# Optimization experiments

Measured on AMD Instinct MI355X. Metric: run time of the kernel, lower is better.

Reference implementation:

```python
import jax, jax.numpy as jnp
import numpy as np

DIM = 768
HEADS = 12
HEAD_DIM = DIM // HEADS
SCALE = HEAD_DIM ** (-0.5)
GAMMA_INIT = 1.0


def _split_heads(x, B, H, Dh):
    # [B, N, C] -> [B, H, N, Dh]
    return x.reshape(B, -1, H, Dh).transpose(0, 2, 1, 3)


def setup_inputs() -> dict:
    key = jax.random.key(0)
    ks = jax.random.split(key, 10)
    B, N, C = 4, 1024, DIM
    w = lambda k: jax.random.normal(k, (C, C), dtype=jnp.float32) * 0.02
    return {
        "fc": jax.random.normal(ks[0], (B, N, C), dtype=jnp.float32),
        "fs": jax.random.normal(ks[1], (B, N, C), dtype=jnp.float32),
        "Wqc": w(ks[2]),
        "Wqs": w(ks[3]),
        "Wkc": w(ks[4]),
        "Wvc": w(ks[5]),
        "Wvs": w(ks[6]),
        "gamma": jnp.ones((HEADS,), dtype=jnp.float32) * GAMMA_INIT,
        "Wpc": w(ks[7]),
        "bpc": jnp.zeros((C,), dtype=jnp.float32),
        "Wps": w(ks[8]),
        "bps": jnp.zeros((C,), dtype=jnp.float32),
    }


def reference(fc, fs, Wqc, Wqs, Wkc, Wvc, Wvs, gamma, Wpc, bpc, Wps, bps):
    B, N, C = fc.shape
    H, Dh = HEADS, HEAD_DIM
    sg = jax.lax.stop_gradient

    qc = _split_heads(fc @ Wqc, B, H, Dh)
    qs = _split_heads(fs @ Wqs, B, H, Dh)
    kc = _split_heads(fc @ Wkc, B, H, Dh)
    vc = _split_heads(fc @ Wvc, B, H, Dh)
    vs = _split_heads(fs @ Wvs, B, H, Dh)

    # content attention: standard scaled QK^T
    attn_c = jnp.einsum("bhnd,bhmd->bhnm", qc, kc) * SCALE
    # semantic attention: L2-normalized self-similarity, per-head gamma
    qs_n = qs / jnp.linalg.norm(qs, axis=-1, keepdims=True)
    attn_s = jnp.einsum("bhnd,bhmd->bhnm", qs_n, qs_n) * gamma[None, :, None, None]

    # double softmax: identical forward values, asymmetric stop-gradients
    attn1 = jax.nn.softmax(attn_c + sg(attn_s), axis=-1)
    attn2 = jax.nn.softmax(sg(attn_c) + attn_s, axis=-1)

    oc = jnp.einsum("bhnm,bhmd->bhnd", attn1, vc).transpose(0, 2, 1, 3).reshape(B, N, C)
    os_ = jnp.einsum("bhnm,bhmd->bhnd", attn2, vs).transpose(0, 2, 1, 3).reshape(B, N, C)

    out_c = oc @ Wpc + bpc
    out_s = os_ @ Wps + bps
    return (out_c, out_s)
```

## Files before the change

kernel.cpp:

```cpp
#include <hip/hip_runtime.h>
#include <cstdint>
#include <cstddef>

#define DEV __device__ __forceinline__

typedef __bf16 v8bf __attribute__((ext_vector_type(8)));
typedef float v4f __attribute__((ext_vector_type(4)));
typedef float f32x16 __attribute__((ext_vector_type(16)));
typedef uint16_t u16;

DEV u16 f2bf(float f) {
    union { __bf16 b; u16 u; } cv;
    cv.b = (__bf16)f;
    return cv.u;
}

DEV uint32_t pkbf(float a, float b) {
    typedef __bf16 bf2v __attribute__((ext_vector_type(2)));
    union { bf2v v; uint32_t u; } c;
    c.v = (bf2v){(__bf16)a, (__bf16)b};
    return c.u;
}

DEV void gload16(void* lds, const void* g) {
    __builtin_amdgcn_global_load_lds(
        (const __attribute__((address_space(1))) unsigned int*)g,
        (__attribute__((address_space(3))) unsigned int*)lds, 16, 0, 0);
}

DEV void wait_vm0() {
    asm volatile("s_waitcnt vmcnt(0)" ::: "memory");
    __builtin_amdgcn_sched_barrier(0);
}

__global__ __launch_bounds__(256) void k_prep(
    const float* __restrict__ fc, const float* __restrict__ fs,
    u16* __restrict__ fcb, u16* __restrict__ fsb,
    const float* __restrict__ w0, const float* __restrict__ w1, const float* __restrict__ w2,
    const float* __restrict__ w3, const float* __restrict__ w4, const float* __restrict__ w5,
    const float* __restrict__ w6, u16* __restrict__ Wt) {
    __shared__ float tl[32][33];
    int bid = blockIdx.x;
    if (bid < 6144) {
        const float* s = (bid < 3072) ? fc : fs;
        u16* d = (bid < 3072) ? fcb : fsb;
        int blk = (bid < 3072) ? bid : (bid - 3072);
        int i = blk * 256 + threadIdx.x;
        float4 v = reinterpret_cast<const float4*>(s)[i];
        ushort4 o;
        o.x = f2bf(v.x); o.y = f2bf(v.y); o.z = f2bf(v.z); o.w = f2bf(v.w);
        reinterpret_cast<ushort4*>(d)[i] = o;
        return;
    }
    int tid = bid - 6144;
    int z = tid / 576, rem = tid % 576;
    const float* W;
    switch (z) {
        case 0: W = w0; break; case 1: W = w1; break; case 2: W = w2; break;
        case 3: W = w3; break; case 4: W = w4; break; case 5: W = w5; break;
        default: W = w6; break;
    }
    int n0 = (rem % 24) * 32, k0 = (rem / 24) * 32;
    int tx = threadIdx.x & 31, ty = threadIdx.x >> 5;
    #pragma unroll
    for (int i = 0; i < 4; ++i)
        tl[ty + i*8][tx] = W[(size_t)(k0 + ty + i*8) * 768 + n0 + tx];
    __syncthreads();
    u16* O = Wt + (size_t)z * 589824;
    #pragma unroll
    for (int i = 0; i < 4; ++i)
        O[(size_t)(n0 + ty + i*8) * 768 + k0 + tx] = f2bf(tl[tx][ty + i*8]);
}

DEV void gemm_main(const u16* __restrict__ A, const u16* __restrict__ W,
                   u16* As, u16* Bs, int m0, int n0, v4f acc[4][4]) {
    const int t = threadIdx.x, lane = t & 63;
    const int wid = t >> 6, wm = wid >> 1, wn = wid & 1;
    const int lr = lane & 15, kg = lane >> 4;
    const int lrow = lane >> 3, lslot = lane & 7;
    const int s = lslot ^ lrow;
    #pragma unroll
    for (int mi = 0; mi < 4; ++mi)
        #pragma unroll
        for (int ni = 0; ni < 4; ++ni) acc[mi][ni] = (v4f){0.f, 0.f, 0.f, 0.f};
    for (int kt = 0; kt < 12; ++kt) {
        int k0 = kt * 64;
        #pragma unroll
        for (int c = 0; c < 4; ++c) {
            int rb = wid * 32 + c * 8;
            int r = rb + lrow;
            gload16((char*)As + rb * 128, A + (size_t)(m0 + r) * 768 + k0 + s * 8);
            gload16((char*)Bs + rb * 128, W + (size_t)(n0 + r) * 768 + k0 + s * 8);
        }
        __syncthreads();
        #pragma unroll
        for (int kk = 0; kk < 2; ++kk) {
            int kb2 = (kk * 32 + kg * 8) * 2;
            v8bf af[4], bfr[4];
            #pragma unroll
            for (int mi = 0; mi < 4; ++mi) {
                int rr = wm * 64 + mi * 16 + lr;
                af[mi] = *reinterpret_cast<const v8bf*>(reinterpret_cast<const char*>(As) + rr * 128 + (kb2 ^ ((rr & 7) << 4)));
            }
            #pragma unroll
            for (int ni = 0; ni < 4; ++ni) {
                int rr = wn * 64 + ni * 16 + lr;
                bfr[ni] = *reinterpret_cast<const v8bf*>(reinterpret_cast<const char*>(Bs) + rr * 128 + (kb2 ^ ((rr & 7) << 4)));
            }
            #pragma unroll
            for (int mi = 0; mi < 4; ++mi)
                #pragma unroll
                for (int ni = 0; ni < 4; ++ni)
                    acc[mi][ni] = __builtin_amdgcn_mfma_f32_16x16x32_bf16(af[mi], bfr[ni], acc[mi][ni], 0, 0, 0);
        }
        __syncthreads();
    }
}

__global__ __launch_bounds__(256) void k_gemm_proj(
    const u16* __restrict__ fcb, const u16* __restrict__ fsb, const u16* __restrict__ Wt,
    u16* __restrict__ qc, u16* __restrict__ kc, u16* __restrict__ vc,
    u16* __restrict__ qs, u16* __restrict__ vs) {
    __shared__ __align__(16) u16 As[8192], Bs[8192];
    const u16* A; const u16* W; u16* O;
    switch (blockIdx.z) {
        case 0:  A = fcb; W = Wt;              O = qc; break;
        case 1:  A = fcb; W = Wt + 589824;     O = kc; break;
        case 2:  A = fcb; W = Wt + 2 * 589824; O = vc; break;
        case 3:  A = fsb; W = Wt + 3 * 589824; O = qs; break;
        default: A = fsb; W = Wt + 4 * 589824; O = vs; break;
    }
    int m0 = blockIdx.y * 128, n0 = blockIdx.x * 128;
    v4f acc[4][4];
    gemm_main(A, W, As, Bs, m0, n0, acc);
    const int lane = threadIdx.x & 63, wid = threadIdx.x >> 6;
    const int wm = wid >> 1, wn = wid & 1, lr = lane & 15, kg = lane >> 4;
    if (blockIdx.z == 0) {
        #pragma unroll
        for (int mi = 0; mi < 4; ++mi)
            #pragma unroll
            for (int ni = 0; ni < 4; ++ni)
                #pragma unroll
                for (int r = 0; r < 4; ++r) acc[mi][ni][r] *= 0.18033688f;
    } else if (blockIdx.z == 3) {
        #pragma unroll
        for (int mi = 0; mi < 4; ++mi)
            #pragma unroll
            for (int r = 0; r < 4; ++r) {
                float ss = 0.f;
                #pragma unroll
                for (int ni = 0; ni < 4; ++ni) ss += acc[mi][ni][r] * acc[mi][ni][r];
                ss += __shfl_xor(ss, 1); ss += __shfl_xor(ss, 2);
                ss += __shfl_xor(ss, 4); ss += __shfl_xor(ss, 8);
                float rs = rsqrtf(ss);
                #pragma unroll
                for (int ni = 0; ni < 4; ++ni) acc[mi][ni][r] *= rs;
            }
    }
    #pragma unroll
    for (int mi = 0; mi < 4; ++mi)
        #pragma unroll
        for (int ni = 0; ni < 4; ++ni)
            #pragma unroll
            for (int r = 0; r < 4; ++r) {
                int rowg = m0 + wm * 64 + mi * 16 + kg * 4 + r;
                int colg = n0 + wn * 64 + ni * 16 + lr;
                O[(size_t)rowg * 768 + colg] = f2bf(acc[mi][ni][r]);
            }
}

__global__ __launch_bounds__(256) void k_gemm_out(
    const u16* __restrict__ ocb, const u16* __restrict__ osb, const u16* __restrict__ Wt,
    const float* __restrict__ bpc, const float* __restrict__ bps, float* __restrict__ out) {
    __shared__ __align__(16) u16 As[8192], Bs[8192];
    const u16* A; const u16* W; const float* bias; float* O;
    if (blockIdx.z == 0) { A = ocb; W = Wt + 5 * 589824; bias = bpc; O = out; }
    else                 { A = osb; W = Wt + 6 * 589824; bias = bps; O = out + 3145728; }
    int m0 = blockIdx.y * 128, n0 = blockIdx.x * 128;
    v4f acc[4][4];
    gemm_main(A, W, As, Bs, m0, n0, acc);
    const int lane = threadIdx.x & 63, wid = threadIdx.x >> 6;
    const int wm = wid >> 1, wn = wid & 1, lr = lane & 15, kg = lane >> 4;
    #pragma unroll
    for (int mi = 0; mi < 4; ++mi)
        #pragma unroll
        for (int ni = 0; ni < 4; ++ni)
            #pragma unroll
            for (int r = 0; r < 4; ++r) {
                int rowg = m0 + wm * 64 + mi * 16 + kg * 4 + r;
                int colg = n0 + wn * 64 + ni * 16 + lr;
                O[(size_t)rowg * 768 + colg] = acc[mi][ni][r] + bias[colg];
            }
}

__global__ __launch_bounds__(256) void k_transpose_v(
    const u16* __restrict__ vc, const u16* __restrict__ vs,
    u16* __restrict__ vcT, u16* __restrict__ vsT) {
    __shared__ u16 tile[64][65];
    const u16* src = blockIdx.z ? vs : vc;
    u16* dst = blockIdx.z ? vsT : vcT;
    int bh = blockIdx.y, b = bh / 12, h = bh % 12;
    int n0 = blockIdx.x * 64;
    int t = threadIdx.x;
    #pragma unroll
    for (int i = 0; i < 16; ++i) {
        int idx = i * 256 + t, n = idx >> 6, d = idx & 63;
        tile[n][d] = src[(size_t)(b * 1024 + n0 + n) * 768 + h * 64 + d];
    }
    __syncthreads();
    #pragma unroll
    for (int i = 0; i < 16; ++i) {
        int idx = i * 256 + t, d = idx >> 6, n = idx & 63;
        dst[(size_t)(bh * 64 + d) * 1024 + n0 + n] = tile[n][d];
    }
}

__global__ __launch_bounds__(256, 2) void k_attn(
    const u16* __restrict__ qc, const u16* __restrict__ kc, const u16* __restrict__ qsn,
    const u16* __restrict__ vcT, const u16* __restrict__ vsT,
    const float* __restrict__ gamma,
    u16* __restrict__ oc, u16* __restrict__ os) {
    __shared__ __align__(16) u16 SH[24576];
    u16* K_s8  = SH;
    u16* Q2_s8 = SH + 4096;
    u16* Vb    = SH + 8192;
    const int t = threadIdx.x, lane = t & 63, w = t >> 6;
    const int lq = lane & 31, hf = lane >> 5;
    const int qg = w >> 1, kvh = w & 1;
    const int lrow = lane >> 3, lslot = lane & 7;
    const int sslot = lslot ^ lrow;

    int lin = blockIdx.y * 16 + blockIdx.x;
    int swz = (lin & 7) * 96 + (lin >> 3);
    const int qb = swz & 15, bh = swz >> 4;
    const int b = bh / 12, h = bh % 12;
    const float gam = gamma[h] * 1.44269504088896340736f;

    const u16* gb; size_t rstride, kmul;
    switch (w) {
        case 0:  gb = kc  + (size_t)b * 786432 + h * 64; rstride = 768;  kmul = 768; break;
        case 1:  gb = qsn + (size_t)b * 786432 + h * 64; rstride = 768;  kmul = 768; break;
        case 2:  gb = vcT + (size_t)bh * 65536;          rstride = 1024; kmul = 1;   break;
        default: gb = vsT + (size_t)bh * 65536;          rstride = 1024; kmul = 1;   break;
    }
    u16* fixdst = (w == 0) ? K_s8 : Q2_s8;

    const u16* qp1 = qc  + (size_t)(b * 1024 + qb * 64 + qg * 32 + lq) * 768 + h * 64 + hf * 8;
    const u16* qp2 = qsn + (size_t)(b * 1024 + qb * 64 + qg * 32 + lq) * 768 + h * 64 + hf * 8;
    v8bf qcB[4], qsB[4];
    #pragma unroll
    for (int s = 0; s < 4; ++s) {
        qcB[s] = *reinterpret_cast<const v8bf*>(qp1 + s * 16);
        qsB[s] = *reinterpret_cast<const v8bf*>(qp2 + s * 16);
    }

    f32x16 ocA[2], osA[2];
    #pragma unroll
    for (int dt = 0; dt < 2; ++dt) {
        #pragma unroll
        for (int r = 0; r < 16; ++r) { ocA[dt][r] = 0.f; osA[dt][r] = 0.f; }
    }
    float lsum = 0.f;

    {
        char* ld = (w < 2) ? (char*)fixdst : (char*)(Vb + (w - 2) * 4096);
        #pragma unroll
        for (int c = 0; c < 8; ++c) {
            int r = c * 8 + lrow;
            int ss = sslot ^ ((c & 1) << 2);
            gload16(ld + c * 1024, gb + (size_t)r * rstride + ss * 8);
        }
    }
    wait_vm0();
    __builtin_amdgcn_s_barrier();

    int cur = 0;
    for (int tile = 0; tile < 16; ++tile) {
        if (tile < 15 && w >= 2) {
            size_t kv1 = (size_t)(tile + 1) * 64;
            char* ld = (char*)(Vb + ((cur ^ 1) * 2 + (w - 2)) * 4096);
            #pragma unroll
            for (int c = 0; c < 8; ++c) {
                int r = c * 8 + lrow;
                int ss = sslot ^ ((c & 1) << 2);
                gload16(ld + c * 1024, gb + kv1 * kmul + (size_t)r * rstride + ss * 8);
            }
        }
        const char* K_s  = (const char*)K_s8;
        const char* Q2_s = (const char*)Q2_s8;
        const char* Vc_s = (const char*)(Vb + (cur * 2 + 0) * 4096);
        const char* Vs_s = (const char*)(Vb + (cur * 2 + 1) * 4096);

        f32x16 ac, as;
        #pragma unroll
        for (int r = 0; r < 16; ++r) { ac[r] = 0.f; as[r] = 0.f; }
        const int rowA = kvh * 32 + lq;
        const int rswA = ((rowA & 7) << 4) ^ (((rowA >> 3) & 1) << 6);
        __builtin_amdgcn_s_setprio(1);
        #pragma unroll
        for (int s = 0; s < 4; ++s) {
            int colb = s * 32 + hf * 16;
            int off = rowA * 128 + (colb ^ rswA);
            v8bf kf  = *reinterpret_cast<const v8bf*>(K_s + off);
            v8bf q2f = *reinterpret_cast<const v8bf*>(Q2_s + off);
            ac = __builtin_amdgcn_mfma_f32_32x32x16_bf16(kf,  qcB[s], ac, 0, 0, 0);
            as = __builtin_amdgcn_mfma_f32_32x32x16_bf16(q2f, qsB[s], as, 0, 0, 0);
        }
        __builtin_amdgcn_s_setprio(0);

        __builtin_amdgcn_s_barrier();
        if (tile < 15 && w < 2) {
            size_t kv1 = (size_t)(tile + 1) * 64;
            #pragma unroll
            for (int c = 0; c < 8; ++c) {
                int r = c * 8 + lrow;
                int ss = sslot ^ ((c & 1) << 2);
                gload16((char*)fixdst + c * 1024, gb + kv1 * kmul + (size_t)r * rstride + ss * 8);
            }
        }

        float p[16];
        #pragma unroll
        for (int r = 0; r < 16; ++r)
            p[r] = __builtin_exp2f(fmaf(gam, as[r], ac[r]));
        lsum += ((p[0]+p[1])+(p[2]+p[3])) + ((p[4]+p[5])+(p[6]+p[7]))
              + ((p[8]+p[9])+(p[10]+p[11])) + ((p[12]+p[13])+(p[14]+p[15]));

        uint32_t A0 = pkbf(p[0], p[1]),  A1 = pkbf(p[2], p[3]);
        uint32_t A2 = pkbf(p[4], p[5]),  A3 = pkbf(p[6], p[7]);
        uint32_t A4 = pkbf(p[8], p[9]),  A5 = pkbf(p[10], p[11]);
        uint32_t A6 = pkbf(p[12], p[13]), A7 = pkbf(p[14], p[15]);
        uint32_t pay0 = hf ? A0 : A2;
        uint32_t pay1 = hf ? A1 : A3;
        uint32_t rec0 = (uint32_t)__shfl_xor((int)pay0, 32);
        uint32_t rec1 = (uint32_t)__shfl_xor((int)pay1, 32);
        uint32_t w0 = hf ? rec0 : A0;
        uint32_t w1 = hf ? rec1 : A1;
        uint32_t w2 = hf ? A2 : rec0;
        uint32_t w3 = hf ? A3 : rec1;
        uint32_t pay2 = hf ? A4 : A6;
        uint32_t pay3 = hf ? A5 : A7;
        uint32_t rec2 = (uint32_t)__shfl_xor((int)pay2, 32);
        uint32_t rec3 = (uint32_t)__shfl_xor((int)pay3, 32);
        uint32_t w4 = hf ? rec2 : A4;
        uint32_t w5 = hf ? rec3 : A5;
        uint32_t w6 = hf ? A6 : rec2;
        uint32_t w7 = hf ? A7 : rec3;
        union { uint32_t u[4]; v8bf v; } pa0, pa1;
        pa0.u[0] = w0; pa0.u[1] = w1; pa0.u[2] = w2; pa0.u[3] = w3;
        pa1.u[0] = w4; pa1.u[1] = w5; pa1.u[2] = w6; pa1.u[3] = w7;

        __builtin_amdgcn_s_setprio(1);
        #pragma unroll
        for (int dt = 0; dt < 2; ++dt) {
            int rowV = dt * 32 + lq;
            int rswV = ((rowV & 7) << 4) ^ (((rowV >> 3) & 1) << 6);
            #pragma unroll
            for (int s = 0; s < 2; ++s) {
                int colb = kvh * 64 + s * 32 + hf * 16;
                int off = rowV * 128 + (colb ^ rswV);
                v8bf vcf = *reinterpret_cast<const v8bf*>(Vc_s + off);
                v8bf vsf = *reinterpret_cast<const v8bf*>(Vs_s + off);
                v8bf ap = s ? pa1.v : pa0.v;
                ocA[dt] = __builtin_amdgcn_mfma_f32_32x32x16_bf16(ap, vcf, ocA[dt], 0, 0, 0);
                osA[dt] = __builtin_amdgcn_mfma_f32_32x32x16_bf16(ap, vsf, osA[dt], 0, 0, 0);
            }
        }
        __builtin_amdgcn_s_setprio(0);

        wait_vm0();
        __builtin_amdgcn_s_barrier();
        cur ^= 1;
    }

    lsum += __shfl_xor(lsum, 32);
    float* red   = reinterpret_cast<float*>(SH);
    float* red_l = red;
    float* red_o = red + 64;
    if (kvh == 1) {
        if (lane < 32) red_l[qg * 32 + lq] = lsum;
        #pragma unroll
        for (int st = 0; st < 2; ++st)
            #pragma unroll
            for (int dt = 0; dt < 2; ++dt)
                #pragma unroll
                for (int r = 0; r < 16; ++r) {
                    int idx = st * 32 + dt * 16 + r;
                    float v = st ? osA[dt][r] : ocA[dt][r];
                    red_o[(qg * 64 + idx) * 64 + lane] = v;
                }
    }
    __syncthreads();
    if (kvh == 0) {
        float ltot = lsum + red_l[qg * 32 + lq];
        float rl = 1.0f / ltot;
        if (lane < 32) red_l[qg * 32 + lq] = rl;
        #pragma unroll
        for (int st = 0; st < 2; ++st)
            #pragma unroll
            for (int dt = 0; dt < 2; ++dt)
                #pragma unroll
                for (int r = 0; r < 16; ++r) {
                    int rowq = (r & 3) + 8 * (r >> 2) + 4 * hf;
                    float rlv = red_l[qg * 32 + rowq];
                    int idx = st * 32 + dt * 16 + r;
                    float own = st ? osA[dt][r] : ocA[dt][r];
                    float v = (own + red_o[(qg * 64 + idx) * 64 + lane]) * rlv;
                    u16* dst = st ? os : oc;
                    dst[(size_t)(b * 1024 + qb * 64 + qg * 32 + rowq) * 768 + h * 64 + dt * 32 + lq] = f2bf(v);
                }
    }
}

extern "C" void kernel_launch(void* const* d_in, const int* in_sizes, int n_in,
                              void* d_out, int out_size, void* d_ws, size_t ws_size,
                              hipStream_t stream) {
    const float* fc    = (const float*)d_in[0];
    const float* fs    = (const float*)d_in[1];
    const float* Wqc   = (const float*)d_in[2];
    const float* Wqs   = (const float*)d_in[3];
    const float* Wkc   = (const float*)d_in[4];
    const float* Wvc   = (const float*)d_in[5];
    const float* Wvs   = (const float*)d_in[6];
    const float* gamma = (const float*)d_in[7];
    const float* Wpc   = (const float*)d_in[8];
    const float* bpc   = (const float*)d_in[9];
    const float* Wps   = (const float*)d_in[10];
    const float* bps   = (const float*)d_in[11];
    float* out = (float*)d_out;

    const size_t NT = 3145728;
    u16* ws  = (u16*)d_ws;
    u16* fcb = ws;
    u16* fsb = fcb + NT;
    u16* Wt  = fsb + NT;
    u16* qc  = Wt + (size_t)7 * 589824;
    u16* kc  = qc + NT;
    u16* vc  = kc + NT;
    u16* qs  = vc + NT;
    u16* vs  = qs + NT;
    u16* vcT = vs + NT;
    u16* vsT = vcT + NT;
    u16* ocb = fcb;
    u16* osb = fsb;

    k_prep<<<10176, 256, 0, stream>>>(fc, fs, fcb, fsb, Wqc, Wkc, Wvc, Wqs, Wvs, Wpc, Wps, Wt);
    k_gemm_proj<<<dim3(6, 32, 5), 256, 0, stream>>>(fcb, fsb, Wt, qc, kc, vc, qs, vs);
    k_transpose_v<<<dim3(16, 48, 2), 256, 0, stream>>>(vc, vs, vcT, vsT);
    k_attn<<<dim3(16, 48), 256, 0, stream>>>(qc, kc, qs, vcT, vsT, gamma, ocb, osb);
    k_gemm_out<<<dim3(6, 32, 2), 256, 0, stream>>>(ocb, osb, Wt, bpc, bps, out);
}
```

Measured before the change: 125.3 us.

## Fuse V transpose into projection GEMM epilogue and swizzle GEMM tile order

The separate V-transpose kernel is removed. The projection GEMM now writes vc and vs directly in transposed [B,H,Dh,N] layout through an LDS staging buffer with vectorized 16-byte stores. This drops one kernel launch and a full read and write of two activation tensors. Both GEMMs also remap block indices with a swizzle for better L2 locality, which adds extra syncs in the V-epilogue blocks.

New measurement: 142.1 us. 13.4% more time.

```diff
diff --git a/kernel.cpp b/kernel.cpp
--- a/kernel.cpp
+++ b/kernel.cpp
@@ -119,68 +119,110 @@
 
 __global__ __launch_bounds__(256) void k_gemm_proj(
     const u16* __restrict__ fcb, const u16* __restrict__ fsb, const u16* __restrict__ Wt,
-    u16* __restrict__ qc, u16* __restrict__ kc, u16* __restrict__ vc,
-    u16* __restrict__ qs, u16* __restrict__ vs) {
-    __shared__ __align__(16) u16 As[8192], Bs[8192];
-    const u16* A; const u16* W; u16* O;
+    u16* __restrict__ qc, u16* __restrict__ kc,
+    u16* __restrict__ qs, u16* __restrict__ vcT, u16* __restrict__ vsT) {
+    __shared__ __align__(16) u16 SH[16384];
+    u16* As = SH;
+    u16* Bs = SH + 8192;
+    const u16* A; const u16* W;
     switch (blockIdx.z) {
-        case 0:  A = fcb; W = Wt;              O = qc; break;
-        case 1:  A = fcb; W = Wt + 589824;     O = kc; break;
-        case 2:  A = fcb; W = Wt + 2 * 589824; O = vc; break;
-        case 3:  A = fsb; W = Wt + 3 * 589824; O = qs; break;
-        default: A = fsb; W = Wt + 4 * 589824; O = vs; break;
-    }
-    int m0 = blockIdx.y * 128, n0 = blockIdx.x * 128;
+        case 0:  A = fcb; W = Wt;              break;
+        case 1:  A = fcb; W = Wt + 589824;     break;
+        case 2:  A = fcb; W = Wt + 2 * 589824; break;
+        case 3:  A = fsb; W = Wt + 3 * 589824; break;
+        default: A = fsb; W = Wt + 4 * 589824; break;
+    }
+    int lin = blockIdx.y * 6 + blockIdx.x;
+    int swz = (lin & 7) * 24 + (lin >> 3);
+    int n0 = (swz % 6) * 128, m0 = (swz / 6) * 128;
+    v4f acc[4][4];
+    gemm_main(A, W, As, Bs, m0, n0, acc);
+    const int t = threadIdx.x;
+    const int lane = t & 63, wid = t >> 6;
+    const int wm = wid >> 1, wn = wid & 1, lr = lane & 15, kg = lane >> 4;
+    if (blockIdx.z == 0) {
+        #pragma unroll
+        for (int mi = 0; mi < 4; ++mi)
+            #pragma unroll
+            for (int ni = 0; ni < 4; ++ni)
+                #pragma unroll
+                for (int r = 0; r < 4; ++r) acc[mi][ni][r] *= 0.18033688f;
+    } else if (blockIdx.z == 3) {
+        #pragma unroll
+        for (int mi = 0; mi < 4; ++mi)
+            #pragma unroll
+            for (int r = 0; r < 4; ++r) {
+                float ss = 0.f;
+                #pragma unroll
+                for (int ni = 0; ni < 4; ++ni) ss += acc[mi][ni][r] * acc[mi][ni][r];
+                ss += __shfl_xor(ss, 1); ss += __shfl_xor(ss, 2);
+                ss += __shfl_xor(ss, 4); ss += __shfl_xor(ss, 8);
+                float rs = rsqrtf(ss);
+                #pragma unroll
+                for (int ni = 0; ni < 4; ++ni) acc[mi][ni][r] *= rs;
+            }
+    }
+    if (blockIdx.z == 2 || blockIdx.z == 4) {
+        u16* T = SH;
+        u16* vT = (blockIdx.z == 2) ? vcT : vsT;
+        const int bq = m0 >> 10, tok0 = m0 & 1023;
+        const int hbase = bq * 12 + n0 / 64;
+        #pragma unroll
+        for (int p = 0; p < 2; ++p) {
+            __syncthreads();
+            if (wn == p) {
+                #pragma unroll
+                for (int mi = 0; mi < 4; ++mi)
+                    #pragma unroll
+                    for (int ni = 0; ni < 4; ++ni) {
+                        int c = ni * 16 + lr;
+                        int rb = wm * 64 + mi * 16 + kg * 4;
+                        ushort4 o;
+                        o.x = f2bf(acc[mi][ni][0]); o.y = f2bf(acc[mi][ni][1]);
+                        o.z = f2bf(acc[mi][ni][2]); o.w = f2bf(acc[mi][ni][3]);
+                        *reinterpret_cast<ushort4*>(&T[c * 136 + rb]) = o;
+                    }
+            }
+            __syncthreads();
+            #pragma unroll
+            for (int it = 0; it < 4; ++it) {
+                int cl = it * 16 + (t >> 4);
+                int r0 = (t & 15) * 8;
+                uint4 v = *reinterpret_cast<const uint4*>(&T[cl * 136 + r0]);
+                *reinterpret_cast<uint4*>(vT + ((size_t)((hbase + p) * 64 + cl)) * 1024 + tok0 + r0) = v;
+            }
+        }
+    } else {
+        u16* O = (blockIdx.z == 0) ? qc : (blockIdx.z == 1) ? kc : qs;
+        #pragma unroll
+        for (int mi = 0; mi < 4; ++mi)
+            #pragma unroll
+            for (int ni = 0; ni < 4; ++ni)
+                #pragma unroll
+                for (int r = 0; r < 4; ++r) {
+                    int rowg = m0 + wm * 64 + mi * 16 + kg * 4 + r;
+                    int colg = n0 + wn * 64 + ni * 16 + lr;
+                    O[(size_t)rowg * 768 + colg] = f2bf(acc[mi][ni][r]);
+                }
+    }
+}
+
+__global__ __launch_bounds__(256) void k_gemm_out(
+    const u16* __restrict__ ocb, const u16* __restrict__ osb, const u16* __restrict__ Wt,
+    const float* __restrict__ bpc, const float* __restrict__ bps, float* __restrict__ out) {
+    __shared__ __align__(16) u16 SH[16384];
+    u16* As = SH;
+    u16* Bs = SH + 8192;
+    const u16* A; const u16* W; const float* bias; float* O;
+    if (blockIdx.z == 0) { A = ocb; W = Wt + 5 * 589824; bias = bpc; O = out; }
+    else                 { A = osb; W = Wt + 6 * 589824; bias = bps; O = out + 3145728; }
+    int lin = blockIdx.y * 6 + blockIdx.x;
+    int swz = (lin & 7) * 24 + (lin >> 3);
+    int n0 = (swz % 6) * 128, m0 = (swz / 6) * 128;
     v4f acc[4][4];
     gemm_main(A, W, As, Bs, m0, n0, acc);
     const int lane = threadIdx.x & 63, wid = threadIdx.x >> 6;
     const int wm = wid >> 1, wn = wid & 1, lr = lane & 15, kg = lane >> 4;
-    if (blockIdx.z == 0) {
-        #pragma unroll
-        for (int mi = 0; mi < 4; ++mi)
-            #pragma unroll
-            for (int ni = 0; ni < 4; ++ni)
-                #pragma unroll
-                for (int r = 0; r < 4; ++r) acc[mi][ni][r] *= 0.18033688f;
-    } else if (blockIdx.z == 3) {
-        #pragma unroll
-        for (int mi = 0; mi < 4; ++mi)
-            #pragma unroll
-            for (int r = 0; r < 4; ++r) {
-                float ss = 0.f;
-                #pragma unroll
-                for (int ni = 0; ni < 4; ++ni) ss += acc[mi][ni][r] * acc[mi][ni][r];
-                ss += __shfl_xor(ss, 1); ss += __shfl_xor(ss, 2);
-                ss += __shfl_xor(ss, 4); ss += __shfl_xor(ss, 8);
-                float rs = rsqrtf(ss);
-                #pragma unroll
-                for (int ni = 0; ni < 4; ++ni) acc[mi][ni][r] *= rs;
-            }
-    }
-    #pragma unroll
-    for (int mi = 0; mi < 4; ++mi)
-        #pragma unroll
-        for (int ni = 0; ni < 4; ++ni)
-            #pragma unroll
-            for (int r = 0; r < 4; ++r) {
-                int rowg = m0 + wm * 64 + mi * 16 + kg * 4 + r;
-                int colg = n0 + wn * 64 + ni * 16 + lr;
-                O[(size_t)rowg * 768 + colg] = f2bf(acc[mi][ni][r]);
-            }
-}
-
-__global__ __launch_bounds__(256) void k_gemm_out(
-    const u16* __restrict__ ocb, const u16* __restrict__ osb, const u16* __restrict__ Wt,
-    const float* __restrict__ bpc, const float* __restrict__ bps, float* __restrict__ out) {
-    __shared__ __align__(16) u16 As[8192], Bs[8192];
-    const u16* A; const u16* W; const float* bias; float* O;
-    if (blockIdx.z == 0) { A = ocb; W = Wt + 5 * 589824; bias = bpc; O = out; }
-    else                 { A = osb; W = Wt + 6 * 589824; bias = bps; O = out + 3145728; }
-    int m0 = blockIdx.y * 128, n0 = blockIdx.x * 128;
-    v4f acc[4][4];
-    gemm_main(A, W, As, Bs, m0, n0, acc);
-    const int lane = threadIdx.x & 63, wid = threadIdx.x >> 6;
-    const int wm = wid >> 1, wn = wid & 1, lr = lane & 15, kg = lane >> 4;
     #pragma unroll
     for (int mi = 0; mi < 4; ++mi)
         #pragma unroll
@@ -191,28 +233,6 @@
                 int colg = n0 + wn * 64 + ni * 16 + lr;
                 O[(size_t)rowg * 768 + colg] = acc[mi][ni][r] + bias[colg];
             }
-}
-
-__global__ __launch_bounds__(256) void k_transpose_v(
-    const u16* __restrict__ vc, const u16* __restrict__ vs,
-    u16* __restrict__ vcT, u16* __restrict__ vsT) {
-    __shared__ u16 tile[64][65];
-    const u16* src = blockIdx.z ? vs : vc;
-    u16* dst = blockIdx.z ? vsT : vcT;
-    int bh = blockIdx.y, b = bh / 12, h = bh % 12;
-    int n0 = blockIdx.x * 64;
-    int t = threadIdx.x;
-    #pragma unroll
-    for (int i = 0; i < 16; ++i) {
-        int idx = i * 256 + t, n = idx >> 6, d = idx & 63;
-        tile[n][d] = src[(size_t)(b * 1024 + n0 + n) * 768 + h * 64 + d];
-    }
-    __syncthreads();
-    #pragma unroll
-    for (int i = 0; i < 16; ++i) {
-        int idx = i * 256 + t, d = idx >> 6, n = idx & 63;
-        dst[(size_t)(bh * 64 + d) * 1024 + n0 + n] = tile[n][d];
-    }
 }
 
 __global__ __launch_bounds__(256, 2) void k_attn(
@@ -445,8 +465,7 @@
     u16* osb = fsb;
 
     k_prep<<<10176, 256, 0, stream>>>(fc, fs, fcb, fsb, Wqc, Wkc, Wvc, Wqs, Wvs, Wpc, Wps, Wt);
-    k_gemm_proj<<<dim3(6, 32, 5), 256, 0, stream>>>(fcb, fsb, Wt, qc, kc, vc, qs, vs);
-    k_transpose_v<<<dim3(16, 48, 2), 256, 0, stream>>>(vc, vs, vcT, vsT);
+    k_gemm_proj<<<dim3(6, 32, 5), 256, 0, stream>>>(fcb, fsb, Wt, qc, kc, qs, vcT, vsT);
     k_attn<<<dim3(16, 48), 256, 0, stream>>>(qc, kc, qs, vcT, vsT, gamma, ocb, osb);
     k_gemm_out<<<dim3(6, 32, 2), 256, 0, stream>>>(ocb, osb, Wt, bpc, bps, out);
 }
```

## Fuse projection GEMMs sharing an input so each A tile is loaded once

Applied to the files above, without the earlier changes.

The projection kernel now computes all weight matrices that share an input (Q/K/V for fc, Q/V for fs) in one block, loading each A tile once and reusing it across up to three weight tiles held in a larger shared buffer. Grid z drops from 5 to 2, which removes redundant A-tile global loads. In exchange each block needs three times the accumulator registers and 64KB of LDS, which lowers occupancy. The grid also shrinks to 384 blocks, possibly underfilling the GPU, and the fs blocks do less work than the fc blocks, leaving the load unbalanced.

Result: slower. 140.6 us (+12.2%).

```diff
diff --git a/kernel.cpp b/kernel.cpp
--- a/kernel.cpp
+++ b/kernel.cpp
@@ -121,52 +121,119 @@
     const u16* __restrict__ fcb, const u16* __restrict__ fsb, const u16* __restrict__ Wt,
     u16* __restrict__ qc, u16* __restrict__ kc, u16* __restrict__ vc,
     u16* __restrict__ qs, u16* __restrict__ vs) {
-    __shared__ __align__(16) u16 As[8192], Bs[8192];
-    const u16* A; const u16* W; u16* O;
-    switch (blockIdx.z) {
-        case 0:  A = fcb; W = Wt;              O = qc; break;
-        case 1:  A = fcb; W = Wt + 589824;     O = kc; break;
-        case 2:  A = fcb; W = Wt + 2 * 589824; O = vc; break;
-        case 3:  A = fsb; W = Wt + 3 * 589824; O = qs; break;
-        default: A = fsb; W = Wt + 4 * 589824; O = vs; break;
+    __shared__ __align__(16) u16 SH[32768];
+    char* AsB = (char*)SH;
+    char* BsB = (char*)(SH + 8192);
+    const int z = blockIdx.z;
+    const int nw = z ? 2 : 3;
+    const u16* A = z ? fsb : fcb;
+    const u16* Wb[3];
+    u16* Ob[3];
+    if (z == 0) {
+        Wb[0] = Wt;              Ob[0] = qc;
+        Wb[1] = Wt + 589824;     Ob[1] = kc;
+        Wb[2] = Wt + 2 * 589824; Ob[2] = vc;
+    } else {
+        Wb[0] = Wt + 3 * 589824; Ob[0] = qs;
+        Wb[1] = Wt + 4 * 589824; Ob[1] = vs;
+        Wb[2] = Wt + 4 * 589824; Ob[2] = vs;
     }
     int m0 = blockIdx.y * 128, n0 = blockIdx.x * 128;
-    v4f acc[4][4];
-    gemm_main(A, W, As, Bs, m0, n0, acc);
-    const int lane = threadIdx.x & 63, wid = threadIdx.x >> 6;
-    const int wm = wid >> 1, wn = wid & 1, lr = lane & 15, kg = lane >> 4;
-    if (blockIdx.z == 0) {
+
+    const int t = threadIdx.x, lane = t & 63;
+    const int wid = t >> 6, wm = wid >> 1, wn = wid & 1;
+    const int lr = lane & 15, kg = lane >> 4;
+    const int lrow = lane >> 3, lslot = lane & 7;
+    const int s = lslot ^ lrow;
+
+    v4f acc[3][4][4];
+    #pragma unroll
+    for (int w = 0; w < 3; ++w)
         #pragma unroll
         for (int mi = 0; mi < 4; ++mi)
             #pragma unroll
+            for (int ni = 0; ni < 4; ++ni) acc[w][mi][ni] = (v4f){0.f, 0.f, 0.f, 0.f};
+
+    for (int kt = 0; kt < 12; ++kt) {
+        int k0 = kt * 64;
+        #pragma unroll
+        for (int c = 0; c < 4; ++c) {
+            int rb = wid * 32 + c * 8;
+            int r = rb + lrow;
+            gload16(AsB + rb * 128, A + (size_t)(m0 + r) * 768 + k0 + s * 8);
+            #pragma unroll
+            for (int w = 0; w < 3; ++w)
+                if (w < nw)
+                    gload16(BsB + w * 16384 + rb * 128, Wb[w] + (size_t)(n0 + r) * 768 + k0 + s * 8);
+        }
+        __syncthreads();
+        #pragma unroll
+        for (int kk = 0; kk < 2; ++kk) {
+            int kb2 = (kk * 32 + kg * 8) * 2;
+            v8bf af[4];
+            #pragma unroll
+            for (int mi = 0; mi < 4; ++mi) {
+                int rr = wm * 64 + mi * 16 + lr;
+                af[mi] = *reinterpret_cast<const v8bf*>(AsB + rr * 128 + (kb2 ^ ((rr & 7) << 4)));
+            }
+            #pragma unroll
+            for (int w = 0; w < 3; ++w) {
+                if (w < nw) {
+                    v8bf bfr[4];
+                    #pragma unroll
+                    for (int ni = 0; ni < 4; ++ni) {
+                        int rr = wn * 64 + ni * 16 + lr;
+                        bfr[ni] = *reinterpret_cast<const v8bf*>(BsB + w * 16384 + rr * 128 + (kb2 ^ ((rr & 7) << 4)));
+                    }
+                    #pragma unroll
+                    for (int mi = 0; mi < 4; ++mi)
+                        #pragma unroll
+                        for (int ni = 0; ni < 4; ++ni)
+                            acc[w][mi][ni] = __builtin_amdgcn_mfma_f32_16x16x32_bf16(af[mi], bfr[ni], acc[w][mi][ni], 0, 0, 0);
+                }
+            }
+        }
+        __syncthreads();
+    }
+
+    if (z == 0) {
+        #pragma unroll
+        for (int mi = 0; mi < 4; ++mi)
+            #pragma unroll
             for (int ni = 0; ni < 4; ++ni)
                 #pragma unroll
-                for (int r = 0; r < 4; ++r) acc[mi][ni][r] *= 0.18033688f;
-    } else if (blockIdx.z == 3) {
+                for (int r = 0; r < 4; ++r) acc[0][mi][ni][r] *= 0.18033688f;
+    } else {
         #pragma unroll
         for (int mi = 0; mi < 4; ++mi)
             #pragma unroll
             for (int r = 0; r < 4; ++r) {
                 float ss = 0.f;
                 #pragma unroll
-                for (int ni = 0; ni < 4; ++ni) ss += acc[mi][ni][r] * acc[mi][ni][r];
+                for (int ni = 0; ni < 4; ++ni) ss += acc[0][mi][ni][r] * acc[0][mi][ni][r];
                 ss += __shfl_xor(ss, 1); ss += __shfl_xor(ss, 2);
                 ss += __shfl_xor(ss, 4); ss += __shfl_xor(ss, 8);
                 float rs = rsqrtf(ss);
                 #pragma unroll
-                for (int ni = 0; ni < 4; ++ni) acc[mi][ni][r] *= rs;
-            }
-    }
-    #pragma unroll
-    for (int mi = 0; mi < 4; ++mi)
-        #pragma unroll
-        for (int ni = 0; ni < 4; ++ni)
-            #pragma unroll
-            for (int r = 0; r < 4; ++r) {
-                int rowg = m0 + wm * 64 + mi * 16 + kg * 4 + r;
-                int colg = n0 + wn * 64 + ni * 16 + lr;
-                O[(size_t)rowg * 768 + colg] = f2bf(acc[mi][ni][r]);
-            }
+                for (int ni = 0; ni < 4; ++ni) acc[0][mi][ni][r] *= rs;
+            }
+    }
+    #pragma unroll
+    for (int w = 0; w < 3; ++w) {
+        if (w < nw) {
+            u16* O = Ob[w];
+            #pragma unroll
+            for (int mi = 0; mi < 4; ++mi)
+                #pragma unroll
+                for (int ni = 0; ni < 4; ++ni)
+                    #pragma unroll
+                    for (int r = 0; r < 4; ++r) {
+                        int rowg = m0 + wm * 64 + mi * 16 + kg * 4 + r;
+                        int colg = n0 + wn * 64 + ni * 16 + lr;
+                        O[(size_t)rowg * 768 + colg] = f2bf(acc[w][mi][ni][r]);
+                    }
+        }
+    }
 }
 
 __global__ __launch_bounds__(256) void k_gemm_out(
@@ -445,7 +512,7 @@
     u16* osb = fsb;
 
     k_prep<<<10176, 256, 0, stream>>>(fc, fs, fcb, fsb, Wqc, Wkc, Wvc, Wqs, Wvs, Wpc, Wps, Wt);
-    k_gemm_proj<<<dim3(6, 32, 5), 256, 0, stream>>>(fcb, fsb, Wt, qc, kc, vc, qs, vs);
+    k_gemm_proj<<<dim3(6, 32, 2), 256, 0, stream>>>(fcb, fsb, Wt, qc, kc, vc, qs, vs);
     k_transpose_v<<<dim3(16, 48, 2), 256, 0, stream>>>(vc, vs, vcT, vsT);
     k_attn<<<dim3(16, 48), 256, 0, stream>>>(qc, kc, qs, vcT, vsT, gamma, ocb, osb);
     k_gemm_out<<<dim3(6, 32, 2), 256, 0, stream>>>(ocb, osb, Wt, bpc, bps, out);
```
